# Performance work log

Hardware: AMD Instinct MI355X
Metric: run time of the kernel (lower is better)

## Reference

```python
import jax, jax.numpy as jnp
import numpy as np

L, B, F, D = 12, 2048, 6144, 768

def setup_inputs() -> dict:
    key = jax.random.key(0)
    k1, k2, k3 = jax.random.split(key, 3)
    acts = jax.random.normal(k1, (L, B, F), dtype=jnp.float32)
    # decoder weights for target layer: stacked per source layer, [L, F, D]
    W = jax.random.normal(k2, (L, F, D), dtype=jnp.float32) * 0.02
    bias = jax.random.normal(k3, (L, D), dtype=jnp.float32) * 0.01
    return {"acts": acts, "W": W, "bias": bias, "layer_idx": 11}

def reference(acts, W, bias, layer_idx):
    # decode(): sum over src_layer <= layer_idx of Linear(a[src], W[src->tgt], b[src->tgt])
    n = layer_idx + 1  # static Python int -> static slice
    a = acts[:n]       # [n, B, F]
    w = W[:n]          # [n, F, D]
    b = bias[:n]       # [n, D]
    # fused accumulation of all per-source-layer GEMMs
    recon = jnp.einsum('lbf,lfd->bd', a, w) + jnp.sum(b, axis=0)  # [B, D]
    return recon
```

## Files before the change

### kernel.cpp

```cpp
#include <hip/hip_runtime.h>
#include <hip/hip_bf16.h>

#define NB 2048
#define NF 6144
#define ND 768
#define BM 256
#define BN 192
#define BK 64
#define SPLITK 2
#define KHALF (NF / SPLITK)
#define NT (KHALF / BK)

#define ABYTES (BM * 128)
#define BBYTES (BN * 128)
#define BUFBYTES (ABYTES + BBYTES)

typedef __attribute__((ext_vector_type(8))) __bf16 bf16x8;
typedef __attribute__((ext_vector_type(4))) float f32x4;

__device__ __forceinline__ char* lds_addr(char* base, int row, int k) {
  const int blk = ((k >> 3) ^ (row & 7) ^ ((row >> 2) & 7)) & 7;
  return base + row * 128 + (blk << 4) + ((k & 7) << 1);
}

#define BAR()                                              \
  do {                                                     \
    asm volatile("s_waitcnt lgkmcnt(0)" ::: "memory");     \
    __builtin_amdgcn_sched_barrier(0);                     \
    __builtin_amdgcn_s_barrier();                          \
    __builtin_amdgcn_sched_barrier(0);                     \
  } while (0)

__global__ __launch_bounds__(256) void bias_init_kernel(
    const float* __restrict__ bias, const int* __restrict__ lidx,
    float* __restrict__ out) {
  int n = lidx[0] + 1;
  int i = blockIdx.x * 256 + threadIdx.x;
  if (i >= NB * ND) return;
  int d = i % ND;
  float s = 0.f;
  for (int l = 0; l < n; ++l) s += bias[l * ND + d];
  out[i] = s;
}

__global__ __launch_bounds__(512, 2) void gemm_kernel(
    const float* __restrict__ acts, const float* __restrict__ W,
    const int* __restrict__ lidx, float* __restrict__ out, int nwg) {
  extern __shared__ char cbuf[];

  const int chunk = nwg >> 3;
  const int swz = (blockIdx.x & 7) * chunk + (blockIdx.x >> 3);
  const int m = swz & 7;
  int rem = swz >> 3;
  const int ks = rem & 1; rem >>= 1;
  const int by = rem & 3; rem >>= 2;
  const int l = rem;
  if (l > lidx[0]) return;

  const int brow = m * BM;
  const int ncol = by * BN;
  const int k0 = ks * KHALF;

  const int tid = threadIdx.x;
  const int lane = tid & 63;
  const int wid = tid >> 6;
  const int wrow = (wid >> 1) * 64;
  const int wcol = (wid & 1) * 96;

  f32x4 acc[4][6];
#pragma unroll
  for (int i = 0; i < 4; ++i)
#pragma unroll
    for (int j = 0; j < 6; ++j) acc[i][j] = (f32x4){0.f, 0.f, 0.f, 0.f};

  const int s_arow = tid >> 3;
  const int s_ak = (tid & 7) * 8;
  const bool bstage = tid < 384;
  const int s_bd = (tid % 48) * 4;
  const int s_bk = (tid / 48) * 8;

  const float* Aptr =
      acts + (size_t)l * NB * NF + (size_t)(brow + s_arow) * NF + k0 + s_ak;
  const float* Bptr =
      W + (size_t)l * NF * ND + (size_t)(k0 + s_bk) * ND + (ncol + s_bd);

  float4 av[4][2];
  float4 bv[8];

  auto LOADS = [&](int kb) {
#pragma unroll
    for (int p = 0; p < 4; ++p) {
      av[p][0] = *(const float4*)(Aptr + (size_t)(64 * p) * NF + kb);
      av[p][1] = *(const float4*)(Aptr + (size_t)(64 * p) * NF + kb + 4);
    }
    if (bstage) {
#pragma unroll
      for (int j = 0; j < 8; ++j)
        bv[j] = *(const float4*)(Bptr + (size_t)(kb + j) * ND);
    }
  };

  auto STORE = [&](int buf) {
    char* cA_ = cbuf + (size_t)buf * BUFBYTES;
    char* cB_ = cA_ + ABYTES;
#pragma unroll
    for (int p = 0; p < 4; ++p) {
      bf16x8 h;
      h[0] = (__bf16)av[p][0].x; h[1] = (__bf16)av[p][0].y;
      h[2] = (__bf16)av[p][0].z; h[3] = (__bf16)av[p][0].w;
      h[4] = (__bf16)av[p][1].x; h[5] = (__bf16)av[p][1].y;
      h[6] = (__bf16)av[p][1].z; h[7] = (__bf16)av[p][1].w;
      *(bf16x8*)lds_addr(cA_, s_arow + 64 * p, s_ak) = h;
    }
    if (bstage) {
#pragma unroll
      for (int dd = 0; dd < 4; ++dd) {
        bf16x8 h;
#pragma unroll
        for (int j = 0; j < 8; ++j) h[j] = (__bf16)bv[j][dd];
        *(bf16x8*)lds_addr(cB_, s_bd + dd, s_bk) = h;
      }
    }
  };

  auto KSTEP = [&](int buf, int s) {
    char* cA_ = cbuf + (size_t)buf * BUFBYTES;
    char* cB_ = cA_ + ABYTES;
    const int kk = s * 32 + (lane >> 4) * 8;
    bf16x8 aF[4], bF[6];
#pragma unroll
    for (int mi = 0; mi < 4; ++mi)
      aF[mi] = *(const bf16x8*)lds_addr(cA_, wrow + mi * 16 + (lane & 15), kk);
#pragma unroll
    for (int ni = 0; ni < 6; ++ni)
      bF[ni] = *(const bf16x8*)lds_addr(cB_, wcol + ni * 16 + (lane & 15), kk);
#pragma unroll
    for (int mi = 0; mi < 4; ++mi)
#pragma unroll
      for (int ni = 0; ni < 6; ++ni)
        acc[mi][ni] = __builtin_amdgcn_mfma_f32_16x16x32_bf16(
            aF[mi], bF[ni], acc[mi][ni], 0, 0, 0);
  };

  LOADS(0);
  STORE(0);
  LOADS(BK);

  for (int t = 0; t < NT; ++t) {
    BAR();
    const int cur = t & 1;
    KSTEP(cur, 0);
    KSTEP(cur, 1);
    if (t + 1 < NT) STORE(cur ^ 1);
    if (t + 2 < NT) LOADS((t + 2) * BK);
  }

  const int orow = brow + wrow + ((lane >> 4) << 2);
  const int ocol = ncol + wcol + (lane & 15);
#pragma unroll
  for (int mi = 0; mi < 4; ++mi)
#pragma unroll
    for (int ni = 0; ni < 6; ++ni)
#pragma unroll
      for (int j = 0; j < 4; ++j)
        atomicAdd(out + (size_t)(orow + mi * 16 + j) * ND + (ocol + ni * 16),
                  acc[mi][ni][j]);
}

extern "C" void kernel_launch(void* const* d_in, const int* in_sizes, int n_in,
                              void* d_out, int out_size, void* d_ws, size_t ws_size,
                              hipStream_t stream) {
  const float* acts = (const float*)d_in[0];
  const float* W    = (const float*)d_in[1];
  const float* bias = (const float*)d_in[2];
  const int*   lidx = (const int*)d_in[3];
  float* out = (float*)d_out;

  const int L = in_sizes[0] / (NB * NF);
  const int nwg = (NB / BM) * SPLITK * (ND / BN) * L;

  hipFuncSetAttribute((const void*)gemm_kernel,
                      hipFuncAttributeMaxDynamicSharedMemorySize,
                      2 * BUFBYTES);

  bias_init_kernel<<<dim3((NB * ND + 255) / 256), 256, 0, stream>>>(bias, lidx, out);
  gemm_kernel<<<dim3(nwg), 512, 2 * BUFBYTES, stream>>>(acts, W, lidx, out, nwg);
}
```

Measured before the change: 575.9 us.

## Restructure GEMM main loop with single-tile prefetch, chunked MFMA and setprio

Global loads for the next K tile are now issued at the top of each iteration instead of two tiles ahead, which cuts register-held prefetch state. LDS fragment reads for B are interleaved with MFMA groups in three chunks, with s_setprio raised around the MFMA bursts and sched_barriers added. The workgroup index decomposition is reordered so that adjacent blocks share the same M tile across N columns, changing L2 reuse of activations. The shorter prefetch distance may expose more global-load latency.

```diff
diff --git a/kernel.cpp b/kernel.cpp
--- a/kernel.cpp
+++ b/kernel.cpp
@@ -8,8 +8,8 @@
 #define BN 192
 #define BK 64
 #define SPLITK 2
-#define KHALF (NF / SPLITK)
-#define NT (KHALF / BK)
+#define KCH (NF / SPLITK)
+#define NTIL (KCH / BK)
 
 #define ABYTES (BM * 128)
 #define BBYTES (BN * 128)
@@ -50,16 +50,16 @@
 
   const int chunk = nwg >> 3;
   const int swz = (blockIdx.x & 7) * chunk + (blockIdx.x >> 3);
-  const int m = swz & 7;
-  int rem = swz >> 3;
+  const int by = swz & 3;
+  int rem = swz >> 2;
+  const int m = rem & 7; rem >>= 3;
   const int ks = rem & 1; rem >>= 1;
-  const int by = rem & 3; rem >>= 2;
   const int l = rem;
   if (l > lidx[0]) return;
 
   const int brow = m * BM;
   const int ncol = by * BN;
-  const int k0 = ks * KHALF;
+  const int k0 = ks * KCH;
 
   const int tid = threadIdx.x;
   const int lane = tid & 63;
@@ -100,9 +100,7 @@
     }
   };
 
-  auto STORE = [&](int buf) {
-    char* cA_ = cbuf + (size_t)buf * BUFBYTES;
-    char* cB_ = cA_ + ABYTES;
+  auto STORE = [&](char* cA_, char* cB_) {
 #pragma unroll
     for (int p = 0; p < 4; ++p) {
       bf16x8 h;
@@ -123,36 +121,52 @@
     }
   };
 
-  auto KSTEP = [&](int buf, int s) {
-    char* cA_ = cbuf + (size_t)buf * BUFBYTES;
-    char* cB_ = cA_ + ABYTES;
-    const int kk = s * 32 + (lane >> 4) * 8;
-    bf16x8 aF[4], bF[6];
-#pragma unroll
-    for (int mi = 0; mi < 4; ++mi)
-      aF[mi] = *(const bf16x8*)lds_addr(cA_, wrow + mi * 16 + (lane & 15), kk);
-#pragma unroll
-    for (int ni = 0; ni < 6; ++ni)
-      bF[ni] = *(const bf16x8*)lds_addr(cB_, wcol + ni * 16 + (lane & 15), kk);
-#pragma unroll
-    for (int mi = 0; mi < 4; ++mi)
-#pragma unroll
-      for (int ni = 0; ni < 6; ++ni)
-        acc[mi][ni] = __builtin_amdgcn_mfma_f32_16x16x32_bf16(
-            aF[mi], bF[ni], acc[mi][ni], 0, 0, 0);
-  };
-
   LOADS(0);
-  STORE(0);
-  LOADS(BK);
-
-  for (int t = 0; t < NT; ++t) {
+  STORE(cbuf, cbuf + ABYTES);
+
+  for (int t = 0; t < NTIL; ++t) {
     BAR();
     const int cur = t & 1;
-    KSTEP(cur, 0);
-    KSTEP(cur, 1);
-    if (t + 1 < NT) STORE(cur ^ 1);
-    if (t + 2 < NT) LOADS((t + 2) * BK);
+    char* rA = cbuf + (size_t)cur * BUFBYTES;
+    char* rB = rA + ABYTES;
+    char* wA = cbuf + (size_t)(cur ^ 1) * BUFBYTES;
+    char* wB = wA + ABYTES;
+
+    if (t + 1 < NTIL) LOADS((t + 1) * BK);
+    __builtin_amdgcn_sched_barrier(0);
+
+    bf16x8 aF[4][2];
+#pragma unroll
+    for (int mi = 0; mi < 4; ++mi)
+#pragma unroll
+      for (int s = 0; s < 2; ++s)
+        aF[mi][s] = *(const bf16x8*)lds_addr(
+            rA, wrow + mi * 16 + (lane & 15), s * 32 + (lane >> 4) * 8);
+
+#pragma unroll
+    for (int p = 0; p < 3; ++p) {
+      bf16x8 bF[2][2];
+#pragma unroll
+      for (int ni = 0; ni < 2; ++ni)
+#pragma unroll
+        for (int s = 0; s < 2; ++s)
+          bF[ni][s] = *(const bf16x8*)lds_addr(
+              rB, wcol + (2 * p + ni) * 16 + (lane & 15),
+              s * 32 + (lane >> 4) * 8);
+      __builtin_amdgcn_s_setprio(1);
+#pragma unroll
+      for (int s = 0; s < 2; ++s)
+#pragma unroll
+        for (int mi = 0; mi < 4; ++mi)
+#pragma unroll
+          for (int ni = 0; ni < 2; ++ni)
+            acc[mi][2 * p + ni] = __builtin_amdgcn_mfma_f32_16x16x32_bf16(
+                aF[mi][s], bF[ni][s], acc[mi][2 * p + ni], 0, 0, 0);
+      __builtin_amdgcn_s_setprio(0);
+      __builtin_amdgcn_sched_barrier(0);
+    }
+
+    if (t + 1 < NTIL) STORE(wA, wB);
   }
 
   const int orow = brow + wrow + ((lane >> 4) << 2);
@@ -177,7 +191,7 @@
   float* out = (float*)d_out;
 
   const int L = in_sizes[0] / (NB * NF);
-  const int nwg = (NB / BM) * SPLITK * (ND / BN) * L;
+  const int nwg = (ND / BN) * (NB / BM) * SPLITK * L;
 
   hipFuncSetAttribute((const void*)gemm_kernel,
                       hipFuncAttributeMaxDynamicSharedMemorySize,
```

New measurement: 475.3 us. 17.5% less time.
